# Kernel tuning notes

Hardware: AMD Instinct MI355X
Metric: run time of the kernel (lower is better)

The kernel has to match this reference:

```python
import jax, jax.numpy as jnp
import numpy as np

N, C, D = 131072, 1024, 64

def setup_inputs() -> dict:
    key = jax.random.key(0)
    k1, k2, k3 = jax.random.split(key, 3)
    inputs = jax.random.normal(k1, (N, D), dtype=jnp.float32)
    centers = jax.random.normal(k2, (C, D), dtype=jnp.float32)
    coefs = jax.random.uniform(k3, (C,), dtype=jnp.float32) / C
    max_avg_distance = jnp.ones((1,), dtype=jnp.float32)
    return {"inputs": inputs, "centers": centers, "coefs": coefs,
            "max_avg_distance": max_avg_distance}

def _pairwise_l2(x, c):
    x2 = jnp.sum(x * x, axis=-1, keepdims=True)          # (N, 1)
    c2 = jnp.sum(c * c, axis=-1)                          # (C,)
    d2 = x2 + c2 - 2.0 * jnp.einsum('nd,cd->nc', x, c)    # (N, C)
    return jnp.sqrt(jnp.maximum(d2, 0.0))

def reference(inputs, centers, coefs, max_avg_distance):
    x = inputs.reshape(inputs.shape[0], -1)               # flatten(inputs, 1)
    distances = _pairwise_l2(x, centers)                  # (N, C)
    c = jnp.abs(coefs)
    s = jnp.sum(c)
    c = jnp.where(s == 0.0, c, c / s)                     # normalize unless sum==0
    weighted_avg = distances @ c                          # (N,)
    return max_avg_distance - weighted_avg                # broadcast (1,)-(N,) -> (N,)
```

## Files before the change

kernel.cpp:

```cpp
#include <hip/hip_runtime.h>
#include <hip/hip_bf16.h>
#include <cstdint>

#define DIM 64
#define NC  1024
#define PF  2

typedef __attribute__((ext_vector_type(8))) __bf16 bf16x8;
typedef __attribute__((ext_vector_type(8))) short short8;
typedef __attribute__((ext_vector_type(4))) float f32x4;
typedef __attribute__((ext_vector_type(4))) unsigned int uint4v;

static __device__ __forceinline__ unsigned short f32_to_bf16_rne(float f) {
    unsigned int u = __builtin_bit_cast(unsigned int, f);
    unsigned int r = u + 0x7FFFu + ((u >> 16) & 1u);
    return (unsigned short)(r >> 16);
}
static __device__ __forceinline__ float bf16_bits_to_f32(unsigned short h) {
    return __builtin_bit_cast(float, (unsigned int)h << 16);
}

__global__ void coef_kernel(const float* __restrict__ coefs,
                            float2* __restrict__ wc2) {
    __shared__ float red[NC];
    const int c = threadIdx.x;
    const float a = fabsf(coefs[c]);
    red[c] = a;
    __syncthreads();
    for (int s = NC / 2; s > 0; s >>= 1) {
        if (c < s) red[c] += red[c + s];
        __syncthreads();
    }
    const float sum = red[0];
    const float w = (sum == 0.0f) ? a : a / sum;
    wc2[c].x = w;
}

__global__ void center_kernel(const float* __restrict__ centers,
                              float2* __restrict__ wc2,
                              short8* __restrict__ bfrag) {
    const int c = blockIdx.x * 64 + threadIdx.x;
    const float4* row = (const float4*)(centers + (size_t)c * DIM);

    float vals[DIM];
    float c2 = 0.0f;
#pragma unroll
    for (int q = 0; q < DIM / 4; ++q) {
        float4 v = row[q];
        vals[q * 4 + 0] = v.x; vals[q * 4 + 1] = v.y;
        vals[q * 4 + 2] = v.z; vals[q * 4 + 3] = v.w;
        c2 = fmaf(v.x, v.x, c2); c2 = fmaf(v.y, v.y, c2);
        c2 = fmaf(v.z, v.z, c2); c2 = fmaf(v.w, v.w, c2);
    }
    const unsigned short hi = f32_to_bf16_rne(c2);
    const unsigned short lo = f32_to_bf16_rne(c2 - bf16_bits_to_f32(hi));
    const unsigned int packed = (unsigned int)hi | ((unsigned int)lo << 16);
    wc2[c].y = __builtin_bit_cast(float, packed);

    const int tile = c >> 4;
    const int colL = c & 15;
#pragma unroll
    for (int kb = 0; kb < 2; ++kb) {
#pragma unroll
        for (int h = 0; h < 4; ++h) {
            short8 p;
#pragma unroll
            for (int j = 0; j < 8; ++j) {
                float v = -2.0f * vals[kb * 32 + h * 8 + j];
                p[j] = (short)f32_to_bf16_rne(v);
            }
            bfrag[(tile * 2 + kb) * 64 + (h * 16 + colL)] = p;
        }
    }
}

__global__ __launch_bounds__(256, 4) void dist_kernel(
    const float* __restrict__ x,
    const float2* __restrict__ wc2,
    const bf16x8* __restrict__ bfrag,
    const float* __restrict__ madp,
    float* __restrict__ out)
{
    const int lane = threadIdx.x & 63;
    const int wave = threadIdx.x >> 6;
    const int lo = lane & 15;
    const int hi = lane >> 4;
    const int pairIdx = wave >> 1;
    const int halfC  = wave & 1;
    const int rowBase = blockIdx.x * 128 + pairIdx * 64;

    __shared__ float part[4][64];

    bf16x8 afrag[4][2];
    f32x4 x2c[4];

#pragma unroll
    for (int g = 0; g < 4; ++g) {
        const int row = rowBase + g * 16 + lo;
        const float* rp = x + (size_t)row * DIM + hi * 8;
        float s2 = 0.0f;
#pragma unroll
        for (int kb = 0; kb < 2; ++kb) {
            float4 v0 = *(const float4*)(rp + kb * 32);
            float4 v1 = *(const float4*)(rp + kb * 32 + 4);
            float vv[8] = {v0.x, v0.y, v0.z, v0.w, v1.x, v1.y, v1.z, v1.w};
            short8 p;
#pragma unroll
            for (int j = 0; j < 8; ++j) {
                s2 = fmaf(vv[j], vv[j], s2);
                p[j] = (short)f32_to_bf16_rne(vv[j]);
            }
            afrag[g][kb] = __builtin_bit_cast(bf16x8, p);
        }
        s2 += __shfl_xor(s2, 16, 64);
        s2 += __shfl_xor(s2, 32, 64);
#pragma unroll
        for (int b = 0; b < 4; ++b)
            x2c[g][b] = __shfl(s2, hi * 4 + b, 64);
    }

    const unsigned int ao = (hi == 0) ? 0x3F803F80u : 0u;
    const bf16x8 afones = __builtin_bit_cast(bf16x8, (uint4v){ao, 0u, 0u, 0u});

    float sum[4][4];
#pragma unroll
    for (int g = 0; g < 4; ++g)
#pragma unroll
        for (int b = 0; b < 4; ++b) sum[g][b] = 0.0f;

    const int tbase = halfC * 32;
    const bf16x8* bp = bfrag + lane;
    const float2* wp = wc2 + lo;

    bf16x8 pb0[PF], pb1[PF];
    float2 pwc[PF];
#pragma unroll
    for (int j = 0; j < PF; ++j) {
        const int t = tbase + j;
        pb0[j] = bp[t * 128];
        pb1[j] = bp[t * 128 + 64];
        pwc[j] = wp[t * 16];
    }

    for (int i = 0; i < 32; i += PF) {
#pragma unroll
        for (int j = 0; j < PF; ++j) {
            const float2 wc = pwc[j];
            const float w = wc.x;
            const unsigned int packed = __builtin_bit_cast(unsigned int, wc.y);
            const bf16x8 bc2 = __builtin_bit_cast(bf16x8, (uint4v){(hi == 0) ? packed : 0u, 0u, 0u, 0u});
            const bf16x8 b0 = pb0[j];
            const bf16x8 b1 = pb1[j];

            {
                const int nxt = i + j + PF;
                const int tn = tbase + ((nxt < 32) ? nxt : 0);
                pb0[j] = bp[tn * 128];
                pb1[j] = bp[tn * 128 + 64];
                pwc[j] = wp[tn * 16];
            }

#pragma unroll
            for (int g = 0; g < 4; ++g) {
                f32x4 acc;
                acc = __builtin_amdgcn_mfma_f32_16x16x32_bf16(afones, bc2, x2c[g], 0, 0, 0);
                acc = __builtin_amdgcn_mfma_f32_16x16x32_bf16(afrag[g][0], b0, acc, 0, 0, 0);
                acc = __builtin_amdgcn_mfma_f32_16x16x32_bf16(afrag[g][1], b1, acc, 0, 0, 0);
#pragma unroll
                for (int b = 0; b < 4; ++b) {
                    float d = __builtin_amdgcn_sqrtf(fabsf(acc[b]));
                    sum[g][b] = fmaf(w, d, sum[g][b]);
                }
            }
        }
    }

#pragma unroll
    for (int g = 0; g < 4; ++g) {
#pragma unroll
        for (int b = 0; b < 4; ++b) {
            float v = sum[g][b];
            v += __shfl_xor(v, 1, 64);
            v += __shfl_xor(v, 2, 64);
            v += __shfl_xor(v, 4, 64);
            v += __shfl_xor(v, 8, 64);
            if (lo == 0) part[wave][g * 16 + hi * 4 + b] = v;
        }
    }
    __syncthreads();

    const int tid = threadIdx.x;
    if (tid < 128) {
        const int p = tid >> 6;
        const int r = tid & 63;
        const float s = part[2 * p][r] + part[2 * p + 1][r];
        out[blockIdx.x * 128 + p * 64 + r] = madp[0] - s;
    }
}

extern "C" void kernel_launch(void* const* d_in, const int* in_sizes, int n_in,
                              void* d_out, int out_size, void* d_ws, size_t ws_size,
                              hipStream_t stream) {
    const float* x       = (const float*)d_in[0];
    const float* centers = (const float*)d_in[1];
    const float* coefs   = (const float*)d_in[2];
    const float* mad     = (const float*)d_in[3];
    float* out = (float*)d_out;

    float2* wc2  = (float2*)d_ws;
    short8* bfrag = (short8*)((char*)d_ws + NC * sizeof(float2));

    const int N = in_sizes[0] / DIM;

    coef_kernel<<<1, NC, 0, stream>>>(coefs, wc2);
    center_kernel<<<NC / 64, 64, 0, stream>>>(centers, wc2, bfrag);
    dist_kernel<<<N / 128, 256, 0, stream>>>(x, wc2, (const bf16x8*)bfrag, mad, out);
}
```

Measured before the change: 46.29 us.

## Stage center fragments through double-buffered LDS via direct global-to-LDS loads

Replaces the per-wave register prefetch of B fragments from global memory with a block-cooperative, double-buffered LDS staging scheme. It uses global_load_lds to copy 16 KB chunks of center fragments, shared by the two waves that work on the same center half. This halves redundant global/L2 traffic and hides latency behind the MFMA work. In exchange it adds 32 KB of LDS per block, which may cut occupancy, and a block-wide barrier every chunk.

Result: slower. 77.57 us (+67.6%).

```diff
diff --git a/kernel.cpp b/kernel.cpp
--- a/kernel.cpp
+++ b/kernel.cpp
@@ -4,7 +4,9 @@
 
 #define DIM 64
 #define NC  1024
-#define PF  2
+
+#define AS1 __attribute__((address_space(1)))
+#define AS3 __attribute__((address_space(3)))
 
 typedef __attribute__((ext_vector_type(8))) __bf16 bf16x8;
 typedef __attribute__((ext_vector_type(8))) short short8;
@@ -18,6 +20,10 @@
 }
 static __device__ __forceinline__ float bf16_bits_to_f32(unsigned short h) {
     return __builtin_bit_cast(float, (unsigned int)h << 16);
+}
+static __device__ __forceinline__ void gload_lds16(const void* g, void* l) {
+    __builtin_amdgcn_global_load_lds((const AS1 unsigned int*)g,
+                                     (AS3 unsigned int*)l, 16, 0, 0);
 }
 
 __global__ void coef_kernel(const float* __restrict__ coefs,
@@ -77,7 +83,7 @@
 __global__ __launch_bounds__(256, 4) void dist_kernel(
     const float* __restrict__ x,
     const float2* __restrict__ wc2,
-    const bf16x8* __restrict__ bfrag,
+    const char* __restrict__ bfragB,
     const float* __restrict__ madp,
     float* __restrict__ out)
 {
@@ -89,10 +95,23 @@
     const int halfC  = wave & 1;
     const int rowBase = blockIdx.x * 128 + pairIdx * 64;
 
+    __shared__ char lbuf[2][16384];
     __shared__ float part[4][64];
 
     bf16x8 afrag[4][2];
     f32x4 x2c[4];
+
+    {
+        const char* span0 = bfragB;
+        const char* span1 = bfragB + 32 * 2048;
+#pragma unroll
+        for (int q = 0; q < 4; ++q) {
+            const int p = wave * 4 + q;
+            const char* src = ((p < 8) ? span0 + p * 1024
+                                       : span1 + (p - 8) * 1024) + lane * 16;
+            gload_lds16(src, &lbuf[0][p * 1024]);
+        }
+    }
 
 #pragma unroll
     for (int g = 0; g < 4; ++g) {
@@ -128,37 +147,45 @@
 #pragma unroll
         for (int b = 0; b < 4; ++b) sum[g][b] = 0.0f;
 
-    const int tbase = halfC * 32;
-    const bf16x8* bp = bfrag + lane;
     const float2* wp = wc2 + lo;
-
-    bf16x8 pb0[PF], pb1[PF];
-    float2 pwc[PF];
-#pragma unroll
-    for (int j = 0; j < PF; ++j) {
-        const int t = tbase + j;
-        pb0[j] = bp[t * 128];
-        pb1[j] = bp[t * 128 + 64];
-        pwc[j] = wp[t * 16];
-    }
-
-    for (int i = 0; i < 32; i += PF) {
-#pragma unroll
-        for (int j = 0; j < PF; ++j) {
-            const float2 wc = pwc[j];
+    float2 wcur[4], wnxt[4];
+#pragma unroll
+    for (int lt = 0; lt < 4; ++lt)
+        wcur[lt] = wp[(halfC * 32 + lt) * 16];
+
+    __syncthreads();
+
+    const int myLds = halfC * 8192;
+
+#pragma unroll 1
+    for (int c = 0; c < 8; ++c) {
+        const int cb = c & 1;
+
+        if (c + 1 < 8) {
+            const char* span0 = bfragB + (c + 1) * 8192;
+            const char* span1 = bfragB + 32 * 2048 + (c + 1) * 8192;
+#pragma unroll
+            for (int q = 0; q < 4; ++q) {
+                const int p = wave * 4 + q;
+                const char* src = ((p < 8) ? span0 + p * 1024
+                                           : span1 + (p - 8) * 1024) + lane * 16;
+                gload_lds16(src, &lbuf[cb ^ 1][p * 1024]);
+            }
+#pragma unroll
+            for (int lt = 0; lt < 4; ++lt)
+                wnxt[lt] = wp[(halfC * 32 + (c + 1) * 4 + lt) * 16];
+        }
+
+#pragma unroll
+        for (int lt = 0; lt < 4; ++lt) {
+            const float2 wc = wcur[lt];
             const float w = wc.x;
             const unsigned int packed = __builtin_bit_cast(unsigned int, wc.y);
-            const bf16x8 bc2 = __builtin_bit_cast(bf16x8, (uint4v){(hi == 0) ? packed : 0u, 0u, 0u, 0u});
-            const bf16x8 b0 = pb0[j];
-            const bf16x8 b1 = pb1[j];
-
-            {
-                const int nxt = i + j + PF;
-                const int tn = tbase + ((nxt < 32) ? nxt : 0);
-                pb0[j] = bp[tn * 128];
-                pb1[j] = bp[tn * 128 + 64];
-                pwc[j] = wp[tn * 16];
-            }
+            const bf16x8 bc2 = __builtin_bit_cast(bf16x8,
+                (uint4v){(hi == 0) ? packed : 0u, 0u, 0u, 0u});
+            const char* tp = &lbuf[cb][myLds + lt * 2048 + lane * 16];
+            const bf16x8 b0 = *(const bf16x8*)tp;
+            const bf16x8 b1 = *(const bf16x8*)(tp + 1024);
 
 #pragma unroll
             for (int g = 0; g < 4; ++g) {
@@ -173,6 +200,10 @@
                 }
             }
         }
+
+        __syncthreads();
+#pragma unroll
+        for (int lt = 0; lt < 4; ++lt) wcur[lt] = wnxt[lt];
     }
 
 #pragma unroll
@@ -207,12 +238,12 @@
     const float* mad     = (const float*)d_in[3];
     float* out = (float*)d_out;
 
-    float2* wc2  = (float2*)d_ws;
+    float2* wc2   = (float2*)d_ws;
     short8* bfrag = (short8*)((char*)d_ws + NC * sizeof(float2));
 
     const int N = in_sizes[0] / DIM;
 
     coef_kernel<<<1, NC, 0, stream>>>(coefs, wc2);
     center_kernel<<<NC / 64, 64, 0, stream>>>(centers, wc2, bfrag);
-    dist_kernel<<<N / 128, 256, 0, stream>>>(x, wc2, (const bf16x8*)bfrag, mad, out);
-}
+    dist_kernel<<<N / 128, 256, 0, stream>>>(x, wc2, (const char*)bfrag, mad, out);
+}
```
